# Performance work log

Measured on AMD Instinct MI355X. Metric: run time of the kernel, lower is better.

The kernel has to match this reference:

```python
import jax, jax.numpy as jnp
import numpy as np

N = 200000
CIN = 64
COUT = 64
K = 9           # taps in a 1x3x3 or 3x1x3 kernel
EPS = 1e-5      # BatchNorm1d eps
SLOPE = 0.01    # LeakyReLU default negative slope


def setup_inputs() -> dict:
    key = jax.random.key(0)
    ks = jax.random.split(key, 7)
    scale = 0.05
    return {
        "x": jax.random.normal(ks[0], (N, CIN), dtype=jnp.float32),
        "w_a0": jax.random.normal(ks[1], (K, CIN, COUT), dtype=jnp.float32) * scale,
        "gamma_a0": jnp.ones((COUT,), jnp.float32),
        "beta_a0": jnp.zeros((COUT,), jnp.float32),
        "w_a1": jax.random.normal(ks[2], (K, COUT, COUT), dtype=jnp.float32) * scale,
        "gamma_a1": jnp.ones((COUT,), jnp.float32),
        "beta_a1": jnp.zeros((COUT,), jnp.float32),
        "w_b0": jax.random.normal(ks[3], (K, CIN, COUT), dtype=jnp.float32) * scale,
        "gamma_b0": jnp.ones((COUT,), jnp.float32),
        "beta_b0": jnp.zeros((COUT,), jnp.float32),
        "w_b1": jax.random.normal(ks[4], (K, COUT, COUT), dtype=jnp.float32) * scale,
        "gamma_b1": jnp.ones((COUT,), jnp.float32),
        "beta_b1": jnp.zeros((COUT,), jnp.float32),
        "idx_133": jax.random.randint(ks[5], (N, K), 0, N),
        "idx_313": jax.random.randint(ks[6], (N, K), 0, N),
    }


def subm_conv(feat, idx, w):
    # gather [N,K,Cin] -> GEMM with [K,Cin,Cout] -> [N,Cout]
    gathered = feat[idx]
    return jnp.einsum('nkc,kcd->nd', gathered, w)


def bn_train(feat, gamma, beta):
    # BatchNorm1d (training mode): biased batch statistics over N
    mean = jnp.mean(feat, axis=0)
    var = jnp.var(feat, axis=0)
    return (feat - mean) * jax.lax.rsqrt(var + EPS) * gamma + beta


def lrelu(feat):
    return jnp.where(feat >= 0, feat, SLOPE * feat)


def reference(x, w_a0, gamma_a0, beta_a0, w_a1, gamma_a1, beta_a1,
              w_b0, gamma_b0, beta_b0, w_b1, gamma_b1, beta_b1,
              idx_133, idx_313):
    # A branch: 1x3x3 -> act -> bn -> 3x1x3 -> act -> bn
    A = subm_conv(x, idx_133, w_a0)
    A = bn_train(lrelu(A), gamma_a0, beta_a0)
    A = subm_conv(A, idx_313, w_a1)
    A = bn_train(lrelu(A), gamma_a1, beta_a1)
    # B0 branch is computed but unused in the original (B = conv_B1(A))
    B0 = bn_train(lrelu(subm_conv(x, idx_313, w_b0)), gamma_b0, beta_b0)  # noqa: F841 (dead, DCE'd)
    # B branch actually uses A per original source
    B = subm_conv(A, idx_133, w_b1)
    B = bn_train(lrelu(B), gamma_b1, beta_b1)
    return A + B
```

## Files before the change

kernel.cpp:

```cpp
#include <hip/hip_runtime.h>

#define N_ROWS 200000
#define NTAP 9
#define BM 128
#define NBLK 1563
#define WSTRIDE 584
#define WCHUNKS 73
#define WT_ELEMS (64*WSTRIDE)
#define TAB_ELEMS ((size_t)N_ROWS*64)
#define VEC8_CNT 1600000

using bf16x8 = __attribute__((ext_vector_type(8))) __bf16;
using f32x4  = __attribute__((ext_vector_type(4))) float;

__device__ __forceinline__ float b2f(unsigned short u) {
  unsigned int x = ((unsigned int)u) << 16;
  return __builtin_bit_cast(float, x);
}
__device__ __forceinline__ unsigned short f2b(float f) {
  unsigned int x = __builtin_bit_cast(unsigned int, f);
  x = x + 0x7fffu + ((x >> 16) & 1u);
  return (unsigned short)(x >> 16);
}
__device__ __forceinline__ void async16(const void* g, void* l) {
  __builtin_amdgcn_global_load_lds((const __attribute__((address_space(1))) unsigned int*)g,
                                   (__attribute__((address_space(3))) unsigned int*)l,
                                   16, 0, 0);
}

__global__ void transp_idx(const int* __restrict__ src, int* __restrict__ dst) {
  int i = blockIdx.x * 256 + threadIdx.x;
  if (i >= N_ROWS * NTAP) return;
  int n = i / NTAP, t = i - n * NTAP;
  dst[t * N_ROWS + n] = src[i];
}

__global__ void prep_x(const float* __restrict__ x, unsigned short* __restrict__ T) {
  int i = blockIdx.x * 256 + threadIdx.x;
  if (i >= VEC8_CNT) return;
  const float4* xv = (const float4*)x + (size_t)i * 2;
  float4 a = xv[0], b = xv[1];
  uint4 o;
  o.x = (unsigned)f2b(a.x) | ((unsigned)f2b(a.y) << 16);
  o.y = (unsigned)f2b(a.z) | ((unsigned)f2b(a.w) << 16);
  o.z = (unsigned)f2b(b.x) | ((unsigned)f2b(b.y) << 16);
  o.w = (unsigned)f2b(b.z) | ((unsigned)f2b(b.w) << 16);
  ((uint4*)T)[i] = o;
}

__global__ void prep_ws(const float* __restrict__ w, const float* __restrict__ stats,
                        unsigned short* __restrict__ wt) {
  int i = blockIdx.x * 256 + threadIdx.x;
  if (i >= WT_ELEMS) return;
  int n = i / WSTRIDE, k = i - n * WSTRIDE;
  float v = 0.f;
  if (k < 576) {
    int tap = k >> 6, ci = k & 63;
    float s = stats ? stats[ci] : 1.0f;
    v = w[tap * 4096 + ci * 64 + n] * s;
  }
  wt[i] = f2b(v);
}

__global__ void prep_bias(const float* __restrict__ w, const float* __restrict__ stats,
                          float* __restrict__ bias) {
  int co = threadIdx.x & 63, part = threadIdx.x >> 6;
  float s = 0.f;
#pragma unroll 4
  for (int e = part; e < 576; e += 4) {
    int tap = e >> 6, ci = e & 63;
    s += stats[64 + ci] * w[tap * 4096 + ci * 64 + co];
  }
  __shared__ float r[4][64];
  r[part][co] = s;
  __syncthreads();
  if (part == 0) bias[co] = r[0][co] + r[1][co] + r[2][co] + r[3][co];
}

__global__ __launch_bounds__(512, 4) void conv_k(
    const unsigned short* __restrict__ T,
    const int* __restrict__ idxT,
    const unsigned short* __restrict__ Wt,
    const float* __restrict__ bias,
    unsigned short* __restrict__ L,
    float* __restrict__ partials)
{
  __shared__ unsigned short Wlds[64][WSTRIDE];
  __shared__ float psum[8][2][64];

  const int tid = threadIdx.x;
  const int w = tid >> 6;
  const int l = tid & 63;
  const int blk = blockIdx.x;
  const int rowbase = blk * BM;
  const int kgrp = l >> 4;

  for (int c = w; c < WCHUNKS; c += 8)
    async16(Wt + c * 512 + l * 8, (unsigned short*)&Wlds[0][0] + c * 512);

  int mrow = rowbase + w * 16 + (l & 15);
  if (mrow > N_ROWS - 1) mrow = N_ROWS - 1;

  int ix[NTAP];
#pragma unroll
  for (int t = 0; t < NTAP; ++t) ix[t] = idxT[t * N_ROWS + mrow];

  __syncthreads();

  const char* Tb = (const char*)T;
  bf16x8 A0[NTAP], A1[NTAP];
#pragma unroll
  for (int t = 0; t < NTAP; ++t) {
    const char* p = Tb + (size_t)((unsigned)ix[t] * 128u) + kgrp * 16;
    A0[t] = *(const bf16x8*)p;
    A1[t] = *(const bf16x8*)(p + 64);
  }
#pragma unroll
  for (int t = 0; t < NTAP; ++t)
    asm volatile("" : "+v"(A0[t]), "+v"(A1[t]));

  float binit[4] = {0.f, 0.f, 0.f, 0.f};
  if (bias) {
#pragma unroll
    for (int f = 0; f < 4; ++f) binit[f] = bias[f * 16 + (l & 15)];
  }

  f32x4 acc[4];
#pragma unroll
  for (int f = 0; f < 4; ++f) acc[f] = (f32x4){binit[f], binit[f], binit[f], binit[f]};

#pragma unroll
  for (int t = 0; t < NTAP; ++t) {
    const unsigned short* wb = &Wlds[l & 15][t * 64 + kgrp * 8];
#pragma unroll
    for (int f = 0; f < 4; ++f) {
      bf16x8 b0 = *(const bf16x8*)(wb + f * 16 * WSTRIDE);
      bf16x8 b1 = *(const bf16x8*)(wb + f * 16 * WSTRIDE + 32);
      acc[f] = __builtin_amdgcn_mfma_f32_16x16x32_bf16(A0[t], b0, acc[f], 0, 0, 0);
      acc[f] = __builtin_amdgcn_mfma_f32_16x16x32_bf16(A1[t], b1, acc[f], 0, 0, 0);
    }
  }

#pragma unroll
  for (int f = 0; f < 4; ++f) {
    int c = f * 16 + (l & 15);
    float sm = 0.f, sq = 0.f;
#pragma unroll
    for (int j = 0; j < 4; ++j) {
      int gr = rowbase + w * 16 + kgrp * 4 + j;
      float v = acc[f][j];
      float y = v >= 0.f ? v : 0.01f * v;
      if (gr < N_ROWS) {
        L[(size_t)gr * 64 + c] = f2b(y);
        sm += y; sq += y * y;
      }
    }
    sm += __shfl_xor(sm, 16); sm += __shfl_xor(sm, 32);
    sq += __shfl_xor(sq, 16); sq += __shfl_xor(sq, 32);
    if (l < 16) { psum[w][0][c] = sm; psum[w][1][c] = sq; }
  }
  __syncthreads();
  if (tid < 128) {
    int j = tid >> 6, c = tid & 63;
    float tot = 0.f;
#pragma unroll
    for (int ww = 0; ww < 8; ++ww) tot += psum[ww][j][c];
    partials[(size_t)(j * 64 + c) * NBLK + blk] = tot;
  }
}

__global__ void reduce_k(const float* __restrict__ part, const float* __restrict__ gamma,
                         const float* __restrict__ beta, float* __restrict__ stats) {
  int c = blockIdx.x, t = threadIdx.x;
  float s = 0.f, q = 0.f;
  for (int b = t; b < NBLK; b += 256) {
    s += part[(size_t)c * NBLK + b];
    q += part[(size_t)(64 + c) * NBLK + b];
  }
#pragma unroll
  for (int m = 1; m < 64; m <<= 1) { s += __shfl_xor(s, m); q += __shfl_xor(q, m); }
  __shared__ float rs[4], rq[4];
  if ((t & 63) == 0) { rs[t >> 6] = s; rq[t >> 6] = q; }
  __syncthreads();
  if (t == 0) {
    float su = rs[0] + rs[1] + rs[2] + rs[3];
    float qu = rq[0] + rq[1] + rq[2] + rq[3];
    float mean = su / (float)N_ROWS;
    float var = qu / (float)N_ROWS - mean * mean;
    float r = rsqrtf(var + 1e-5f);
    float sc = gamma[c] * r;
    stats[c] = sc;
    stats[64 + c] = beta[c] - mean * sc;
  }
}

__global__ void final_k(const unsigned short* __restrict__ L2v,
                        const unsigned short* __restrict__ L3v,
                        const float* __restrict__ st2, const float* __restrict__ st3,
                        float* __restrict__ out) {
  int i = blockIdx.x * 256 + threadIdx.x;
  if (i >= VEC8_CNT) return;
  uint4 av = ((const uint4*)L2v)[i];
  uint4 yv = ((const uint4*)L3v)[i];
  int c0 = (i & 7) * 8;
  unsigned va[4] = {av.x, av.y, av.z, av.w};
  unsigned vy[4] = {yv.x, yv.y, yv.z, yv.w};
  float o[8];
#pragma unroll
  for (int h = 0; h < 4; ++h) {
    int c = c0 + 2 * h;
    float a0 = b2f((unsigned short)(va[h] & 0xffff));
    float a1 = b2f((unsigned short)(va[h] >> 16));
    float y0 = b2f((unsigned short)(vy[h] & 0xffff));
    float y1 = b2f((unsigned short)(vy[h] >> 16));
    o[2 * h]     = a0 * st2[c]     + st2[64 + c]     + y0 * st3[c]     + st3[64 + c];
    o[2 * h + 1] = a1 * st2[c + 1] + st2[64 + c + 1] + y1 * st3[c + 1] + st3[64 + c + 1];
  }
  float4* ov = (float4*)(out + (size_t)i * 8);
  ov[0] = make_float4(o[0], o[1], o[2], o[3]);
  ov[1] = make_float4(o[4], o[5], o[6], o[7]);
}

extern "C" void kernel_launch(void* const* d_in, const int* in_sizes, int n_in,
                              void* d_out, int out_size, void* d_ws, size_t ws_size,
                              hipStream_t stream) {
  (void)in_sizes; (void)n_in; (void)out_size; (void)ws_size;
  const float* x    = (const float*)d_in[0];
  const float* w_a0 = (const float*)d_in[1];
  const float* g_a0 = (const float*)d_in[2];
  const float* b_a0 = (const float*)d_in[3];
  const float* w_a1 = (const float*)d_in[4];
  const float* g_a1 = (const float*)d_in[5];
  const float* b_a1 = (const float*)d_in[6];
  const float* w_b1 = (const float*)d_in[10];
  const float* g_b1 = (const float*)d_in[11];
  const float* b_b1 = (const float*)d_in[12];
  const int* idx133 = (const int*)d_in[13];
  const int* idx313 = (const int*)d_in[14];
  float* out = (float*)d_out;

  char* ws = (char*)d_ws;
  unsigned short* wt0 = (unsigned short*)ws;
  unsigned short* wt1 = wt0 + WT_ELEMS;
  unsigned short* wt2 = wt1 + WT_ELEMS;
  unsigned short* Tx  = wt2 + WT_ELEMS;
  unsigned short* L1  = Tx + TAB_ELEMS;
  unsigned short* L2  = L1 + TAB_ELEMS;
  unsigned short* L3  = Tx;
  int* it133 = (int*)(L2 + TAB_ELEMS);
  int* it313 = it133 + N_ROWS * NTAP;
  float* part = (float*)(it313 + N_ROWS * NTAP);
  float* st1 = part + 2 * 64 * NBLK;
  float* st2 = st1 + 128;
  float* st3 = st2 + 128;
  float* bias1 = st3 + 128;
  float* bias2 = bias1 + 64;

  transp_idx<<<(N_ROWS * NTAP + 255) / 256, 256, 0, stream>>>(idx133, it133);
  transp_idx<<<(N_ROWS * NTAP + 255) / 256, 256, 0, stream>>>(idx313, it313);
  prep_x<<<(VEC8_CNT + 255) / 256, 256, 0, stream>>>(x, Tx);
  prep_ws<<<(WT_ELEMS + 255) / 256, 256, 0, stream>>>(w_a0, nullptr, wt0);

  conv_k<<<NBLK, 512, 0, stream>>>(Tx, it133, wt0, nullptr, L1, part);
  reduce_k<<<64, 256, 0, stream>>>(part, g_a0, b_a0, st1);
  prep_ws<<<(WT_ELEMS + 255) / 256, 256, 0, stream>>>(w_a1, st1, wt1);
  prep_bias<<<1, 256, 0, stream>>>(w_a1, st1, bias1);

  conv_k<<<NBLK, 512, 0, stream>>>(L1, it313, wt1, bias1, L2, part);
  reduce_k<<<64, 256, 0, stream>>>(part, g_a1, b_a1, st2);
  prep_ws<<<(WT_ELEMS + 255) / 256, 256, 0, stream>>>(w_b1, st2, wt2);
  prep_bias<<<1, 256, 0, stream>>>(w_b1, st2, bias2);

  conv_k<<<NBLK, 512, 0, stream>>>(L2, it133, wt2, bias2, L3, part);
  reduce_k<<<64, 256, 0, stream>>>(part, g_b1, b_b1, st3);

  final_k<<<(VEC8_CNT + 255) / 256, 256, 0, stream>>>(L2, L3, st2, st3, out);
}
```

Measured before the change: 223.3 us.

## Drop index transposes and fuse weight/bias prep into BN reduction kernels

Removes the two index-transpose kernels and has the conv kernel read the row-major [N,9] index array directly, at the cost of strided per-lane index loads. Merges the weight conversion for the first conv with precomputed tap-summed weights into one prep kernel. Folds the next layer's scaled-weight packing and bias computation into the BN statistics reduction, using an atomic counter so the last block computes the bias. This cuts the launch count and the index traffic, but adds cross-block atomics and threadfence ordering, and it drops the asm barrier that held the gathers in registers.

Measured after the change: 242.8 us. +8.7%, slower.

```diff
diff --git a/kernel.cpp b/kernel.cpp
--- a/kernel.cpp
+++ b/kernel.cpp
@@ -28,11 +28,28 @@
                                    16, 0, 0);
 }
 
-__global__ void transp_idx(const int* __restrict__ src, int* __restrict__ dst) {
+__global__ void prep_all(const float* __restrict__ wa0, const float* __restrict__ wa1,
+                         const float* __restrict__ wb1, unsigned short* __restrict__ wt0,
+                         float* __restrict__ wsum1, float* __restrict__ wsum2,
+                         int* __restrict__ ctr) {
   int i = blockIdx.x * 256 + threadIdx.x;
-  if (i >= N_ROWS * NTAP) return;
-  int n = i / NTAP, t = i - n * NTAP;
-  dst[t * N_ROWS + n] = src[i];
+  if (i < WT_ELEMS) {
+    int n = i / WSTRIDE, k = i - n * WSTRIDE;
+    float v = 0.f;
+    if (k < 576) { int tap = k >> 6, ci = k & 63; v = wa0[tap * 4096 + ci * 64 + n]; }
+    wt0[i] = f2b(v);
+  } else if (i < WT_ELEMS + 8192) {
+    int j = i - WT_ELEMS;
+    const float* w = j < 4096 ? wa1 : wb1;
+    float* o = j < 4096 ? wsum1 : wsum2;
+    int e = j & 4095;
+    float s = 0.f;
+#pragma unroll
+    for (int t = 0; t < NTAP; ++t) s += w[t * 4096 + e];
+    o[e] = s;
+  } else if (i < WT_ELEMS + 8192 + 2) {
+    ctr[i - (WT_ELEMS + 8192)] = 0;
+  }
 }
 
 __global__ void prep_x(const float* __restrict__ x, unsigned short* __restrict__ T) {
@@ -48,38 +65,9 @@
   ((uint4*)T)[i] = o;
 }
 
-__global__ void prep_ws(const float* __restrict__ w, const float* __restrict__ stats,
-                        unsigned short* __restrict__ wt) {
-  int i = blockIdx.x * 256 + threadIdx.x;
-  if (i >= WT_ELEMS) return;
-  int n = i / WSTRIDE, k = i - n * WSTRIDE;
-  float v = 0.f;
-  if (k < 576) {
-    int tap = k >> 6, ci = k & 63;
-    float s = stats ? stats[ci] : 1.0f;
-    v = w[tap * 4096 + ci * 64 + n] * s;
-  }
-  wt[i] = f2b(v);
-}
-
-__global__ void prep_bias(const float* __restrict__ w, const float* __restrict__ stats,
-                          float* __restrict__ bias) {
-  int co = threadIdx.x & 63, part = threadIdx.x >> 6;
-  float s = 0.f;
-#pragma unroll 4
-  for (int e = part; e < 576; e += 4) {
-    int tap = e >> 6, ci = e & 63;
-    s += stats[64 + ci] * w[tap * 4096 + ci * 64 + co];
-  }
-  __shared__ float r[4][64];
-  r[part][co] = s;
-  __syncthreads();
-  if (part == 0) bias[co] = r[0][co] + r[1][co] + r[2][co] + r[3][co];
-}
-
 __global__ __launch_bounds__(512, 4) void conv_k(
     const unsigned short* __restrict__ T,
-    const int* __restrict__ idxT,
+    const int* __restrict__ idx,
     const unsigned short* __restrict__ Wt,
     const float* __restrict__ bias,
     unsigned short* __restrict__ L,
@@ -101,9 +89,10 @@
   int mrow = rowbase + w * 16 + (l & 15);
   if (mrow > N_ROWS - 1) mrow = N_ROWS - 1;
 
+  const int* ip = idx + (size_t)mrow * NTAP;
   int ix[NTAP];
 #pragma unroll
-  for (int t = 0; t < NTAP; ++t) ix[t] = idxT[t * N_ROWS + mrow];
+  for (int t = 0; t < NTAP; ++t) ix[t] = ip[t];
 
   __syncthreads();
 
@@ -115,9 +104,6 @@
     A0[t] = *(const bf16x8*)p;
     A1[t] = *(const bf16x8*)(p + 64);
   }
-#pragma unroll
-  for (int t = 0; t < NTAP; ++t)
-    asm volatile("" : "+v"(A0[t]), "+v"(A1[t]));
 
   float binit[4] = {0.f, 0.f, 0.f, 0.f};
   if (bias) {
@@ -169,8 +155,11 @@
   }
 }
 
-__global__ void reduce_k(const float* __restrict__ part, const float* __restrict__ gamma,
-                         const float* __restrict__ beta, float* __restrict__ stats) {
+__global__ void mk_next(const float* __restrict__ part, const float* __restrict__ gamma,
+                        const float* __restrict__ beta, float* __restrict__ stats,
+                        const float* __restrict__ wnext, const float* __restrict__ wsum,
+                        unsigned short* __restrict__ wtnext, float* __restrict__ biasnext,
+                        int* __restrict__ ctr) {
   int c = blockIdx.x, t = threadIdx.x;
   float s = 0.f, q = 0.f;
   for (int b = t; b < NBLK; b += 256) {
@@ -180,6 +169,8 @@
 #pragma unroll
   for (int m = 1; m < 64; m <<= 1) { s += __shfl_xor(s, m); q += __shfl_xor(q, m); }
   __shared__ float rs[4], rq[4];
+  __shared__ float ssc;
+  __shared__ int lastFlag;
   if ((t & 63) == 0) { rs[t >> 6] = s; rq[t >> 6] = q; }
   __syncthreads();
   if (t == 0) {
@@ -191,6 +182,27 @@
     float sc = gamma[c] * r;
     stats[c] = sc;
     stats[64 + c] = beta[c] - mean * sc;
+    ssc = sc;
+  }
+  __syncthreads();
+  if (!wnext) return;
+
+  float sc = ssc;
+  for (int e = t; e < 576; e += 256) {
+    int tap = e >> 6, co = e & 63;
+    wtnext[co * WSTRIDE + tap * 64 + c] = f2b(wnext[tap * 4096 + c * 64 + co] * sc);
+  }
+
+  __threadfence();
+  if (t == 0) lastFlag = (atomicAdd(ctr, 1) == 63);
+  __syncthreads();
+  if (lastFlag && t < 64) {
+    __threadfence();
+    const volatile float* vst = stats;
+    float b = 0.f;
+#pragma unroll 8
+    for (int ci = 0; ci < 64; ++ci) b += vst[64 + ci] * wsum[ci * 64 + t];
+    biasnext[t] = b;
   }
 }
 
@@ -247,32 +259,29 @@
   unsigned short* L1  = Tx + TAB_ELEMS;
   unsigned short* L2  = L1 + TAB_ELEMS;
   unsigned short* L3  = Tx;
-  int* it133 = (int*)(L2 + TAB_ELEMS);
-  int* it313 = it133 + N_ROWS * NTAP;
-  float* part = (float*)(it313 + N_ROWS * NTAP);
+  float* part = (float*)(L2 + TAB_ELEMS);
   float* st1 = part + 2 * 64 * NBLK;
   float* st2 = st1 + 128;
   float* st3 = st2 + 128;
   float* bias1 = st3 + 128;
   float* bias2 = bias1 + 64;
-
-  transp_idx<<<(N_ROWS * NTAP + 255) / 256, 256, 0, stream>>>(idx133, it133);
-  transp_idx<<<(N_ROWS * NTAP + 255) / 256, 256, 0, stream>>>(idx313, it313);
+  float* wsum1 = bias2 + 64;
+  float* wsum2 = wsum1 + 4096;
+  int* ctr = (int*)(wsum2 + 4096);
+
+  prep_all<<<(WT_ELEMS + 8192 + 2 + 255) / 256, 256, 0, stream>>>(
+      w_a0, w_a1, w_b1, wt0, wsum1, wsum2, ctr);
   prep_x<<<(VEC8_CNT + 255) / 256, 256, 0, stream>>>(x, Tx);
-  prep_ws<<<(WT_ELEMS + 255) / 256, 256, 0, stream>>>(w_a0, nullptr, wt0);
-
-  conv_k<<<NBLK, 512, 0, stream>>>(Tx, it133, wt0, nullptr, L1, part);
-  reduce_k<<<64, 256, 0, stream>>>(part, g_a0, b_a0, st1);
-  prep_ws<<<(WT_ELEMS + 255) / 256, 256, 0, stream>>>(w_a1, st1, wt1);
-  prep_bias<<<1, 256, 0, stream>>>(w_a1, st1, bias1);
-
-  conv_k<<<NBLK, 512, 0, stream>>>(L1, it313, wt1, bias1, L2, part);
-  reduce_k<<<64, 256, 0, stream>>>(part, g_a1, b_a1, st2);
-  prep_ws<<<(WT_ELEMS + 255) / 256, 256, 0, stream>>>(w_b1, st2, wt2);
-  prep_bias<<<1, 256, 0, stream>>>(w_b1, st2, bias2);
-
-  conv_k<<<NBLK, 512, 0, stream>>>(L2, it133, wt2, bias2, L3, part);
-  reduce_k<<<64, 256, 0, stream>>>(part, g_b1, b_b1, st3);
+
+  conv_k<<<NBLK, 512, 0, stream>>>(Tx, idx133, wt0, nullptr, L1, part);
+  mk_next<<<64, 256, 0, stream>>>(part, g_a0, b_a0, st1, w_a1, wsum1, wt1, bias1, ctr);
+
+  conv_k<<<NBLK, 512, 0, stream>>>(L1, idx313, wt1, bias1, L2, part);
+  mk_next<<<64, 256, 0, stream>>>(part, g_a1, b_a1, st2, w_b1, wsum2, wt2, bias2, ctr + 1);
+
+  conv_k<<<NBLK, 512, 0, stream>>>(L2, idx133, wt2, bias2, L3, part);
+  mk_next<<<64, 256, 0, stream>>>(part, g_b1, b_b1, st3, nullptr, nullptr, nullptr, nullptr,
+                                  nullptr);
 
   final_k<<<(VEC8_CNT + 255) / 256, 256, 0, stream>>>(L2, L3, st2, st3, out);
 }
```
